# Optimization experiments

Hardware: AMD Instinct MI355X
Metric: run time of the kernel (lower is better)

The kernel has to match this reference:

```python
import jax, jax.numpy as jnp
import numpy as np

POOLED_H, POOLED_W = 7, 7
SPATIAL_SCALE = 0.25
SAMPLING_RATIO = 2  # fixed > 0, so exactly sr x sr grid points per bin


def setup_inputs() -> dict:
    key = jax.random.key(0)
    k1, k2, k3, k4 = jax.random.split(key, 4)
    N, C, H, W = 4, 256, 200, 200
    K = 1000
    feature = jax.random.normal(k1, (N, C, H, W), dtype=jnp.float32)
    # rois in this module's convention: (batch_idx, y1, x1, y2, x2) in IMAGE coords
    # (image is 800x800 since spatial_scale = 0.25 -> 200x200 feature map)
    b = jax.random.randint(k2, (K,), 0, N).astype(jnp.float32)
    yx1 = jax.random.uniform(k3, (K, 2), minval=0.0, maxval=700.0)
    wh = jax.random.uniform(k4, (K, 2), minval=20.0, maxval=100.0)
    yx2 = jnp.clip(yx1 + wh, 0.0, 800.0)
    rois = jnp.concatenate([b[:, None], yx1[:, :1], yx1[:, 1:], yx2[:, :1], yx2[:, 1:]], axis=1)
    return {"feature": feature, "rois": rois}


def _axis_prep(coord, size):
    """coord: [K, G] continuous sample coords along one axis of length `size`.
    Returns low/high integer indices and (masked) lerp weights, matching the
    torchvision/detectron bilinear_interpolate edge handling (aligned=False)."""
    valid = ((coord >= -1.0) & (coord <= size)).astype(coord.dtype)
    c = jnp.maximum(coord, 0.0)
    c0 = jnp.minimum(jnp.floor(c).astype(jnp.int32), size - 1)
    c1 = jnp.minimum(c0 + 1, size - 1)
    l = jnp.where(c0 >= size - 1, 0.0, c - c0.astype(c.dtype))
    h = 1.0 - l
    return c0, c1, l * valid, h * valid


def _roi_align_2d(feature, rois_tv):
    # rois_tv: [K,5] = (batch, x1, y1, x2, y2) in torchvision order
    N, C, H, W = feature.shape
    K = rois_tv.shape[0]
    sr = SAMPLING_RATIO
    GH, GW = POOLED_H * sr, POOLED_W * sr
    b = rois_tv[:, 0].astype(jnp.int32)
    x1 = rois_tv[:, 1] * SPATIAL_SCALE
    y1 = rois_tv[:, 2] * SPATIAL_SCALE
    x2 = rois_tv[:, 3] * SPATIAL_SCALE
    y2 = rois_tv[:, 4] * SPATIAL_SCALE
    roi_w = jnp.maximum(x2 - x1, 1.0)
    roi_h = jnp.maximum(y2 - y1, 1.0)
    bin_w = roi_w / POOLED_W  # [K]
    bin_h = roi_h / POOLED_H
    # per-axis sample grid offsets (in units of bins): bin + (i+0.5)/sr
    gw = jnp.arange(GW) // sr + (jnp.arange(GW) % sr + 0.5) / sr  # [GW]
    gh = jnp.arange(GH) // sr + (jnp.arange(GH) % sr + 0.5) / sr  # [GH]
    xs = x1[:, None] + gw[None, :] * bin_w[:, None]  # [K, GW]
    ys = y1[:, None] + gh[None, :] * bin_h[:, None]  # [K, GH]
    x0, x1i, lx, hx = _axis_prep(xs, W)
    y0, y1i, ly, hy = _axis_prep(ys, H)

    def gather(yc, xc):
        # -> [K, GH, GW, C]
        return feature[b[:, None, None], :, yc[:, :, None], xc[:, None, :]]

    # bilinear: weights are separable in y and x
    wy_hi = hy[:, :, None, None]  # [K,GH,1,1]
    wy_lo = ly[:, :, None, None]
    wx_hi = hx[:, None, :, None]  # [K,1,GW,1]
    wx_lo = lx[:, None, :, None]
    val = (wy_hi * wx_hi * gather(y0, x0)
           + wy_hi * wx_lo * gather(y0, x1i)
           + wy_lo * wx_hi * gather(y1i, x0)
           + wy_lo * wx_lo * gather(y1i, x1i))  # [K, GH, GW, C]
    # average the sr x sr samples per bin
    out = val.reshape(K, POOLED_H, sr, POOLED_W, sr, C).mean(axis=(2, 4))
    return jnp.transpose(out, (0, 3, 1, 2))  # [K, C, PH, PW]


def reference(feature, rois):
    # module forward: permute (b, y1, x1, y2, x2) -> (b, x1, y1, x2, y2)
    rois_tv = rois[:, jnp.array([0, 2, 1, 4, 3])]
    return _roi_align_2d(feature, rois_tv)
```

## Files before the change

### kernel.cpp

```cpp
#include <hip/hip_runtime.h>


constexpr int POOLED = 7;
constexpr int C_DIM = 256;
constexpr int H_DIM = 200;
constexpr int W_DIM = 200;
constexpr float SCALE = 0.25f;

constexpr int PROWS = 27;
constexpr int PSTR  = 36;

__global__ __launch_bounds__(256, 8) void roi_align_v4(
    const float* __restrict__ feat,
    const float* __restrict__ rois,
    float* __restrict__ out)
{
    __shared__ float patch[4][PROWS][PSTR];

    const int k    = blockIdx.x;
    const int cg   = blockIdx.y;
    const int w    = threadIdx.x >> 6;
    const int lane = threadIdx.x & 63;
    const int c    = cg * 4 + w;

    const float* r = rois + (size_t)k * 5;
    const int   n  = (int)r[0];
    const float y1 = r[1] * SCALE;
    const float x1 = r[2] * SCALE;
    const float y2 = r[3] * SCALE;
    const float x2 = r[4] * SCALE;

    const float bw = fmaxf(x2 - x1, 1.0f) * (1.0f / POOLED);
    const float bh = fmaxf(y2 - y1, 1.0f) * (1.0f / POOLED);

    const int rx0 = (int)fmaf(0.25f, bw, x1);
    const int ry0 = (int)fmaf(0.25f, bh, y1);
    const int rx1 = (int)fmaf(6.75f, bw, x1);
    const int ry1 = (int)fmaf(6.75f, bh, y1);
    const int rx0a = rx0 & ~3;
    const int R    = ry1 - ry0 + 1;
    const int w4   = ((rx1 + 1 - rx0a) >> 2) + 1;

    const float* plane = feat + ((size_t)n * C_DIM + c) * (size_t)(H_DIM * W_DIM);
    {
        const int ly = lane >> 3;
        const int lx = lane & 7;
        const int col4 = rx0a + lx * 4;
        const int lb   = min(col4, W_DIM - 4);
        const bool hi  = col4 > W_DIM - 4;
        const bool colon = (lx < w4);

        float4 v[4];
        bool   on[4];
        #pragma unroll
        for (int i = 0; i < 4; ++i) {
            const int rr = ly + 8 * i;
            on[i] = colon && (rr <= R);
            if (on[i]) {
                const int srow = min(ry0 + rr, H_DIM - 1);
                v[i] = *reinterpret_cast<const float4*>(plane + srow * W_DIM + lb);
            }
        }
        #pragma unroll
        for (int i = 0; i < 4; ++i) {
            if (on[i]) {
                float4 t = v[i];
                if (hi) { t.x = t.w; t.y = t.w; t.z = t.w; }
                *reinterpret_cast<float4*>(&patch[w][ly + 8 * i][lx * 4]) = t;
            }
        }
    }

    if (lane < POOLED * POOLED) {
        const int ph = (lane * 37) >> 8;
        const int pw = lane - ph * 7;

        float lxw[2], hxw[2], lyw[2], hyw[2];
        int   xr[2], yr[2];
        #pragma unroll
        for (int i = 0; i < 2; ++i) {
            const float fi = 0.25f + 0.5f * (float)i;
            float xs = fmaf((float)pw + fi, bw, x1);
            int   a0 = (int)xs;
            lxw[i] = xs - (float)a0;
            hxw[i] = 1.0f - lxw[i];
            xr[i]  = a0 - rx0a;
            float ys = fmaf((float)ph + fi, bh, y1);
            int   b0 = (int)ys;
            lyw[i] = ys - (float)b0;
            hyw[i] = 1.0f - lyw[i];
            yr[i]  = b0 - ry0;
        }

        float acc = 0.0f;
        #pragma unroll
        for (int iy = 0; iy < 2; ++iy) {
            #pragma unroll
            for (int ix = 0; ix < 2; ++ix) {
                const int y0 = yr[iy], x0 = xr[ix];
                const float v00 = patch[w][y0][x0];
                const float v01 = patch[w][y0][x0 + 1];
                const float v10 = patch[w][y0 + 1][x0];
                const float v11 = patch[w][y0 + 1][x0 + 1];
                const float t0 = fmaf(lxw[ix], v01, hxw[ix] * v00);
                const float t1 = fmaf(lxw[ix], v11, hxw[ix] * v10);
                acc = fmaf(hyw[iy], t0, fmaf(lyw[iy], t1, acc));
            }
        }

        out[((size_t)k * C_DIM + c) * (POOLED * POOLED) + lane] = acc * 0.25f;
    }
}

extern "C" void kernel_launch(void* const* d_in, const int* in_sizes, int n_in,
                              void* d_out, int out_size, void* d_ws, size_t ws_size,
                              hipStream_t stream) {
    const float* feature = (const float*)d_in[0];
    const float* rois    = (const float*)d_in[1];
    float* out = (float*)d_out;

    int K = in_sizes[1] / 5;
    dim3 grid(K, C_DIM / 4);
    roi_align_v4<<<grid, 256, 0, stream>>>(feature, rois, out);
}
```

Measured before the change: 83.02 us.

## Process two channels per wave and precompute ROI params in a prep kernel

Each wave now loads and interpolates two channel planes instead of one, halving the grid and amortizing ROI setup across more work, with all eight float4 loads issued before the LDS stores. A separate small kernel precomputes per-ROI parameters into workspace so the main kernel reads one aligned struct. The bilinear corner weights are precomputed, with the 1/4 averaging folded into them. The cost is a doubled LDS footprint per block (launch bounds lowered to 5), more registers, and an extra kernel launch.

```diff
diff --git a/kernel.cpp b/kernel.cpp
--- a/kernel.cpp
+++ b/kernel.cpp
@@ -5,68 +5,101 @@
 constexpr int C_DIM = 256;
 constexpr int H_DIM = 200;
 constexpr int W_DIM = 200;
+constexpr int HW    = H_DIM * W_DIM;
 constexpr float SCALE = 0.25f;
 
 constexpr int PROWS = 27;
 constexpr int PSTR  = 36;
 
-__global__ __launch_bounds__(256, 8) void roi_align_v4(
+struct alignas(16) RoiParams {
+    float bw, bh, x1, y1;
+    int   n, rx0a, ry0, rw;
+};
+
+__device__ __forceinline__ RoiParams compute_params(const float* __restrict__ rois, int k)
+{
+    const float* r = rois + (size_t)k * 5;
+    RoiParams p;
+    const float y1 = r[1] * SCALE;
+    const float x1 = r[2] * SCALE;
+    const float y2 = r[3] * SCALE;
+    const float x2 = r[4] * SCALE;
+    p.bw = fmaxf(x2 - x1, 1.0f) * (1.0f / POOLED);
+    p.bh = fmaxf(y2 - y1, 1.0f) * (1.0f / POOLED);
+    p.x1 = x1;
+    p.y1 = y1;
+    p.n  = (int)r[0];
+    const int rx0 = (int)fmaf(0.25f, p.bw, x1);
+    const int ry0 = (int)fmaf(0.25f, p.bh, y1);
+    const int rx1 = (int)fmaf(6.75f, p.bw, x1);
+    const int ry1 = (int)fmaf(6.75f, p.bh, y1);
+    p.rx0a = rx0 & ~3;
+    p.ry0  = ry0;
+    const int R  = ry1 - ry0 + 1;
+    const int w4 = ((rx1 + 1 - p.rx0a) >> 2) + 1;
+    p.rw = (R << 8) | w4;
+    return p;
+}
+
+__global__ __launch_bounds__(64) void roi_prep(
+    const float* __restrict__ rois, RoiParams* __restrict__ pp, int K)
+{
+    const int k = blockIdx.x * 64 + threadIdx.x;
+    if (k < K) pp[k] = compute_params(rois, k);
+}
+
+template <bool USE_TABLE>
+__global__ __launch_bounds__(256, 5) void roi_align_v5(
     const float* __restrict__ feat,
     const float* __restrict__ rois,
+    const RoiParams* __restrict__ pp,
     float* __restrict__ out)
 {
-    __shared__ float patch[4][PROWS][PSTR];
+    __shared__ float patch[8][PROWS][PSTR];
 
     const int k    = blockIdx.x;
     const int cg   = blockIdx.y;
     const int w    = threadIdx.x >> 6;
     const int lane = threadIdx.x & 63;
-    const int c    = cg * 4 + w;
+    const int c0   = cg * 8 + w * 2;
 
-    const float* r = rois + (size_t)k * 5;
-    const int   n  = (int)r[0];
-    const float y1 = r[1] * SCALE;
-    const float x1 = r[2] * SCALE;
-    const float y2 = r[3] * SCALE;
-    const float x2 = r[4] * SCALE;
+    const RoiParams p = USE_TABLE ? pp[k] : compute_params(rois, k);
+    const int R  = p.rw >> 8;
+    const int w4 = p.rw & 255;
 
-    const float bw = fmaxf(x2 - x1, 1.0f) * (1.0f / POOLED);
-    const float bh = fmaxf(y2 - y1, 1.0f) * (1.0f / POOLED);
-
-    const int rx0 = (int)fmaf(0.25f, bw, x1);
-    const int ry0 = (int)fmaf(0.25f, bh, y1);
-    const int rx1 = (int)fmaf(6.75f, bw, x1);
-    const int ry1 = (int)fmaf(6.75f, bh, y1);
-    const int rx0a = rx0 & ~3;
-    const int R    = ry1 - ry0 + 1;
-    const int w4   = ((rx1 + 1 - rx0a) >> 2) + 1;
-
-    const float* plane = feat + ((size_t)n * C_DIM + c) * (size_t)(H_DIM * W_DIM);
+    const float* plane0 = feat + ((size_t)p.n * C_DIM + c0) * (size_t)HW;
     {
         const int ly = lane >> 3;
         const int lx = lane & 7;
-        const int col4 = rx0a + lx * 4;
+        const int col4 = p.rx0a + lx * 4;
         const int lb   = min(col4, W_DIM - 4);
         const bool hi  = col4 > W_DIM - 4;
-        const bool colon = (lx < w4);
+        const bool con = lx < w4;
 
-        float4 v[4];
-        bool   on[4];
+        int  roff[4];
+        bool on[4];
         #pragma unroll
         for (int i = 0; i < 4; ++i) {
             const int rr = ly + 8 * i;
-            on[i] = colon && (rr <= R);
-            if (on[i]) {
-                const int srow = min(ry0 + rr, H_DIM - 1);
-                v[i] = *reinterpret_cast<const float4*>(plane + srow * W_DIM + lb);
-            }
+            on[i] = con && (rr <= R);
+            roff[i] = min(p.ry0 + rr, H_DIM - 1) * W_DIM + lb;
         }
+        float4 v0[4], v1[4];
+        #pragma unroll
+        for (int i = 0; i < 4; ++i)
+            if (on[i]) v0[i] = *reinterpret_cast<const float4*>(plane0 + roff[i]);
+        #pragma unroll
+        for (int i = 0; i < 4; ++i)
+            if (on[i]) v1[i] = *reinterpret_cast<const float4*>(plane0 + HW + roff[i]);
         #pragma unroll
         for (int i = 0; i < 4; ++i) {
             if (on[i]) {
-                float4 t = v[i];
+                float4 t = v0[i];
                 if (hi) { t.x = t.w; t.y = t.w; t.z = t.w; }
-                *reinterpret_cast<float4*>(&patch[w][ly + 8 * i][lx * 4]) = t;
+                *reinterpret_cast<float4*>(&patch[w * 2 + 0][ly + 8 * i][lx * 4]) = t;
+                t = v1[i];
+                if (hi) { t.x = t.w; t.y = t.w; t.z = t.w; }
+                *reinterpret_cast<float4*>(&patch[w * 2 + 1][ly + 8 * i][lx * 4]) = t;
             }
         }
     }
@@ -75,40 +108,52 @@
         const int ph = (lane * 37) >> 8;
         const int pw = lane - ph * 7;
 
-        float lxw[2], hxw[2], lyw[2], hyw[2];
+        float wx[2][2], wy[2][2];
         int   xr[2], yr[2];
         #pragma unroll
         for (int i = 0; i < 2; ++i) {
             const float fi = 0.25f + 0.5f * (float)i;
-            float xs = fmaf((float)pw + fi, bw, x1);
+            float xs = fmaf((float)pw + fi, p.bw, p.x1);
             int   a0 = (int)xs;
-            lxw[i] = xs - (float)a0;
-            hxw[i] = 1.0f - lxw[i];
-            xr[i]  = a0 - rx0a;
-            float ys = fmaf((float)ph + fi, bh, y1);
+            const float l = xs - (float)a0;
+            wx[i][0] = 1.0f - l;
+            wx[i][1] = l;
+            xr[i] = a0 - p.rx0a;
+            float ys = fmaf((float)ph + fi, p.bh, p.y1);
             int   b0 = (int)ys;
-            lyw[i] = ys - (float)b0;
-            hyw[i] = 1.0f - lyw[i];
-            yr[i]  = b0 - ry0;
+            const float m = ys - (float)b0;
+            wy[i][0] = (1.0f - m) * 0.25f;
+            wy[i][1] = m * 0.25f;
+            yr[i] = b0 - p.ry0;
         }
+        float cw[2][2][2][2];
+        #pragma unroll
+        for (int iy = 0; iy < 2; ++iy)
+            #pragma unroll
+            for (int ix = 0; ix < 2; ++ix)
+                #pragma unroll
+                for (int dy = 0; dy < 2; ++dy)
+                    #pragma unroll
+                    for (int dx = 0; dx < 2; ++dx)
+                        cw[iy][ix][dy][dx] = wy[iy][dy] * wx[ix][dx];
 
-        float acc = 0.0f;
+        const size_t obase = ((size_t)k * C_DIM + c0) * (POOLED * POOLED) + lane;
         #pragma unroll
-        for (int iy = 0; iy < 2; ++iy) {
+        for (int pc = 0; pc < 2; ++pc) {
+            float acc = 0.0f;
             #pragma unroll
-            for (int ix = 0; ix < 2; ++ix) {
-                const int y0 = yr[iy], x0 = xr[ix];
-                const float v00 = patch[w][y0][x0];
-                const float v01 = patch[w][y0][x0 + 1];
-                const float v10 = patch[w][y0 + 1][x0];
-                const float v11 = patch[w][y0 + 1][x0 + 1];
-                const float t0 = fmaf(lxw[ix], v01, hxw[ix] * v00);
-                const float t1 = fmaf(lxw[ix], v11, hxw[ix] * v10);
-                acc = fmaf(hyw[iy], t0, fmaf(lyw[iy], t1, acc));
+            for (int iy = 0; iy < 2; ++iy) {
+                #pragma unroll
+                for (int ix = 0; ix < 2; ++ix) {
+                    const int y0 = yr[iy], x0 = xr[ix];
+                    acc = fmaf(cw[iy][ix][0][0], patch[w * 2 + pc][y0][x0],         acc);
+                    acc = fmaf(cw[iy][ix][0][1], patch[w * 2 + pc][y0][x0 + 1],     acc);
+                    acc = fmaf(cw[iy][ix][1][0], patch[w * 2 + pc][y0 + 1][x0],     acc);
+                    acc = fmaf(cw[iy][ix][1][1], patch[w * 2 + pc][y0 + 1][x0 + 1], acc);
+                }
             }
+            out[obase + (size_t)pc * (POOLED * POOLED)] = acc;
         }
-
-        out[((size_t)k * C_DIM + c) * (POOLED * POOLED) + lane] = acc * 0.25f;
     }
 }
 
@@ -120,6 +165,13 @@
     float* out = (float*)d_out;
 
     int K = in_sizes[1] / 5;
-    dim3 grid(K, C_DIM / 4);
-    roi_align_v4<<<grid, 256, 0, stream>>>(feature, rois, out);
+    dim3 grid(K, C_DIM / 8);
+
+    if (ws_size >= sizeof(RoiParams) * (size_t)K) {
+        RoiParams* pp = (RoiParams*)d_ws;
+        roi_prep<<<(K + 63) / 64, 64, 0, stream>>>(rois, pp, K);
+        roi_align_v5<true><<<grid, 256, 0, stream>>>(feature, rois, pp, out);
+    } else {
+        roi_align_v5<false><<<grid, 256, 0, stream>>>(feature, rois, nullptr, out);
+    }
 }
```

Result: slower. 88.77 us (+6.9%).
